# Optimization experiments

Hardware: AMD Instinct MI355X
Metric: run time of the kernel (lower is better)

Reference implementation:

```python
import jax, jax.numpy as jnp
import numpy as np
import math

HIDDEN = 1024
HEADS = 16
HEAD = HIDDEN // HEADS  # 64
SCALE_BASE = 512.0


def _gammas(heads):
    # 1 - exp(linspace(log(1/32), log(1/512), heads))
    return 1.0 - jnp.exp(jnp.linspace(math.log(1.0 / 32.0), math.log(1.0 / 512.0), heads))


def _xpos(x, downscale):
    # x: [B, H, S, d]  (same head_size d for every head -> shared tables)
    S, d = x.shape[2], x.shape[3]
    half = d // 2
    base_scale = (jnp.arange(0, d, 2, dtype=jnp.float32) + 0.4 * d) / (1.4 * d)  # [half]
    pos = jnp.arange(S, dtype=jnp.float32)
    scale = base_scale[None, :] ** (pos / SCALE_BASE)[:, None]  # [S, half]
    if downscale:
        scale = 1.0 / scale
    inv_freq = 1.0 / (10000.0 ** (jnp.arange(half, dtype=jnp.float32) / half))
    sinusoid = pos[:, None] * inv_freq[None, :]  # [S, half]
    # duplicate-interleave (each column repeated twice)
    sin = jnp.repeat(jnp.sin(sinusoid) * scale, 2, axis=-1)  # [S, d]
    cos = jnp.repeat(jnp.cos(sinusoid) * scale, 2, axis=-1)  # [S, d]
    x1 = x[..., ::2]
    x2 = x[..., 1::2]
    rot = jnp.stack([-x2, x1], axis=-1).reshape(x.shape)  # rotate_every_two
    return x * cos + rot * sin


def _decay_mask(S, gammas):
    # D[h, n, m] = gamma_h^(n-m) for n >= m else 0
    n = jnp.arange(S)[:, None]
    m = jnp.arange(S)[None, :]
    diff = (n - m).astype(jnp.float32)
    mask = (n >= m)
    pw = jnp.maximum(diff, 0.0)[None, :, :]  # avoid overflow on negative diffs
    return jnp.where(mask[None, :, :], gammas[:, None, None] ** pw, 0.0)  # [H, S, S]


def retention_forward(Q, K, V):
    B, S, _ = Q.shape
    # split heads: [B, S, HIDDEN] -> [B, H, S, HEAD]
    def split(x, hd):
        return x.reshape(B, S, HEADS, hd).transpose(0, 2, 1, 3)
    q = _xpos(split(Q, HEAD), downscale=False)
    k = _xpos(split(K, HEAD), downscale=True)
    v = split(V, HEAD)
    D = _decay_mask(S, _gammas(HEADS).astype(Q.dtype))  # [H, S, S]
    scores = jnp.einsum('bhsd,bhtd->bhst', q, k) * D[None]
    out = jnp.einsum('bhst,bhtd->bhsd', scores, v)
    return out.transpose(0, 2, 1, 3).reshape(B, S, HEADS * HEAD)


def setup_inputs() -> dict:
    key = jax.random.key(0)
    kq, kk, kv = jax.random.split(key, 3)
    B, S = 2, 2048
    return {
        'Q': jax.random.normal(kq, (B, S, HIDDEN), dtype=jnp.float32),
        'K': jax.random.normal(kk, (B, S, HIDDEN), dtype=jnp.float32),
        'V': jax.random.normal(kv, (B, S, HIDDEN), dtype=jnp.float32),
    }


def reference(Q, K, V):
    return retention_forward(Q, K, V)
```

## Files before the change

kernel.cpp:

```cpp
#include <hip/hip_runtime.h>
#include <hip/hip_bf16.h>
#include <math.h>

#define B_  2
#define S_  2048
#define H_  16
#define D_  64

typedef __attribute__((ext_vector_type(8))) short bf16x8_t;
typedef __attribute__((ext_vector_type(4))) float f32x4_t;

__device__ __forceinline__ unsigned short f2bf(float f) {
    __hip_bfloat16 h = __float2bfloat16(f);
    return __builtin_bit_cast(unsigned short, h);
}
__device__ __forceinline__ float bf2f(unsigned short u) {
    unsigned int x = ((unsigned int)u) << 16;
    return __builtin_bit_cast(float, x);
}

__device__ __forceinline__ void rotpair(int i, float pos, float& cs_s, float& sn_s, bool down) {
    float bsc  = (2.0f * (float)i + 25.6f) / 89.6f;
    float xsc  = exp2f(log2f(bsc) * pos * (1.0f / 512.0f));
    float invf = exp2f(-(float)i * (13.287712379549449f / 32.0f));
    float ang  = pos * invf;
    float kq = rintf(ang * 0.15915494309189535f);
    float rr = fmaf(kq, -6.2831853071795865f, ang);
    float sn = sinf(rr), cs = cosf(rr);
    float sc = down ? (1.0f / xsc) : xsc;
    cs_s = cs * sc; sn_s = sn * sc;
}

__global__ __launch_bounds__(256) void gkv_kernel(const float* __restrict__ K,
                                                  const float* __restrict__ V,
                                                  unsigned short* __restrict__ kb,
                                                  unsigned short* __restrict__ vt,
                                                  unsigned short* __restrict__ Gg) {
    __shared__ float tileF[64 * 65];
    __shared__ __align__(16) unsigned short vtile[64 * 72];
    __shared__ __align__(16) unsigned short ktile[64 * 72];
    int t = threadIdx.x;
    int idx = blockIdx.x;
    int bh = idx >> 5, j = idx & 31;
    int b = bh >> 4, hh = bh & 15;
    int s0 = j * 64;
    int d = t >> 2, c = t & 3;

    float lnv = -3.4657359027997265f + (float)hh * (-0.18483924814931874f);
    float l2g = log2f(1.0f - expf(lnv));

    float4 vreg[4];
#pragma unroll
    for (int it = 0; it < 4; ++it) {
        int f  = it * 256 + t;
        int sl = f >> 4, d4 = f & 15;
        vreg[it] = *(const float4*)(V + ((long)(b * S_ + s0 + sl)) * 1024 + hh * 64 + d4 * 4);
    }
    float kreg[4][4];
#pragma unroll
    for (int it = 0; it < 4; ++it) {
        int f  = it * 256 + t;
        int sl = f >> 4, d4 = f & 15;
        float pos = (float)(s0 + sl);
        long a = ((long)(b * S_ + s0 + sl)) * 1024 + hh * 64 + d4 * 4;
        float4 xk = *(const float4*)(K + a);
        float gsi = exp2f(-pos * l2g);
        float c0, s0f, c1, s1f;
        rotpair(2 * d4 + 0, pos, c0, s0f, true);
        rotpair(2 * d4 + 1, pos, c1, s1f, true);
        float ck0 = c0 * gsi, sk0 = s0f * gsi;
        float ck1 = c1 * gsi, sk1 = s1f * gsi;
        kreg[it][0] = xk.x * ck0 - xk.y * sk0;
        kreg[it][1] = xk.y * ck0 + xk.x * sk0;
        kreg[it][2] = xk.z * ck1 - xk.w * sk1;
        kreg[it][3] = xk.w * ck1 + xk.z * sk1;
        *(uint2*)(kb + a) = make_uint2((unsigned)f2bf(kreg[it][0]) | ((unsigned)f2bf(kreg[it][1]) << 16),
                                       (unsigned)f2bf(kreg[it][2]) | ((unsigned)f2bf(kreg[it][3]) << 16));
    }
#pragma unroll
    for (int it = 0; it < 4; ++it) {
        int f  = it * 256 + t;
        int sl = f >> 4, d4 = f & 15;
        tileF[sl * 65 + d4 * 4 + 0] = vreg[it].x;
        tileF[sl * 65 + d4 * 4 + 1] = vreg[it].y;
        tileF[sl * 65 + d4 * 4 + 2] = vreg[it].z;
        tileF[sl * 65 + d4 * 4 + 3] = vreg[it].w;
    }
    __syncthreads();
    {
        unsigned int pk[8];
#pragma unroll
        for (int jj = 0; jj < 8; ++jj) {
            float f0 = tileF[(c * 16 + 2 * jj + 0) * 65 + d];
            float f1 = tileF[(c * 16 + 2 * jj + 1) * 65 + d];
            pk[jj] = (unsigned int)f2bf(f0) | ((unsigned int)f2bf(f1) << 16);
        }
        uint4 u0 = make_uint4(pk[0], pk[1], pk[2], pk[3]);
        uint4 u1 = make_uint4(pk[4], pk[5], pk[6], pk[7]);
        ((uint4*)&vtile[d * 72 + c * 16])[0] = u0;
        ((uint4*)&vtile[d * 72 + c * 16 + 8])[0] = u1;
        unsigned short* outp = vt + ((long)(bh * 64 + d)) * S_ + s0 + c * 16;
        ((uint4*)outp)[0] = u0;
        ((uint4*)outp)[1] = u1;
    }
    __syncthreads();
#pragma unroll
    for (int it = 0; it < 4; ++it) {
        int f  = it * 256 + t;
        int sl = f >> 4, d4 = f & 15;
        tileF[sl * 65 + d4 * 4 + 0] = kreg[it][0];
        tileF[sl * 65 + d4 * 4 + 1] = kreg[it][1];
        tileF[sl * 65 + d4 * 4 + 2] = kreg[it][2];
        tileF[sl * 65 + d4 * 4 + 3] = kreg[it][3];
    }
    __syncthreads();
    {
        unsigned int pk[8];
#pragma unroll
        for (int jj = 0; jj < 8; ++jj) {
            float f0 = tileF[(c * 16 + 2 * jj + 0) * 65 + d];
            float f1 = tileF[(c * 16 + 2 * jj + 1) * 65 + d];
            pk[jj] = (unsigned int)f2bf(f0) | ((unsigned int)f2bf(f1) << 16);
        }
        ((uint4*)&ktile[d * 72 + c * 16])[0] = make_uint4(pk[0], pk[1], pk[2], pk[3]);
        ((uint4*)&ktile[d * 72 + c * 16 + 8])[0] = make_uint4(pk[4], pk[5], pk[6], pk[7]);
    }
    __syncthreads();

    int w = t >> 6, lane = t & 63, quad = lane >> 4, l16 = lane & 15;
    f32x4_t accS[4];
#pragma unroll
    for (int dkt = 0; dkt < 4; ++dkt) accS[dkt] = (f32x4_t){0.f, 0.f, 0.f, 0.f};

    bf16x8_t aV[2], bK[4][2];
#pragma unroll
    for (int sst = 0; sst < 2; ++sst)
        aV[sst] = *(const bf16x8_t*)&vtile[(w * 16 + l16) * 72 + sst * 32 + quad * 8];
#pragma unroll
    for (int dkt = 0; dkt < 4; ++dkt)
#pragma unroll
        for (int sst = 0; sst < 2; ++sst)
            bK[dkt][sst] = *(const bf16x8_t*)&ktile[(dkt * 16 + l16) * 72 + sst * 32 + quad * 8];
#pragma unroll
    for (int dkt = 0; dkt < 4; ++dkt)
#pragma unroll
        for (int sst = 0; sst < 2; ++sst)
            accS[dkt] = __builtin_amdgcn_mfma_f32_16x16x32_bf16(aV[sst], bK[dkt][sst], accS[dkt], 0, 0, 0);

    unsigned short* Gp = Gg + (long)idx * 4096;
#pragma unroll
    for (int dkt = 0; dkt < 4; ++dkt)
#pragma unroll
        for (int r = 0; r < 4; ++r)
            Gp[(w * 16 + quad * 4 + r) * 64 + dkt * 16 + l16] = f2bf(accS[dkt][r]);
}

__global__ __launch_bounds__(256) void scan_kernel(const unsigned short* __restrict__ Gg,
                                                   unsigned short* __restrict__ Sg) {
    int tid = blockIdx.x * 256 + threadIdx.x;
    int bh  = tid >> 12;
    int e   = tid & 4095;
    long base = ((long)bh * 32) * 4096 + e;
    float acc = 0.0f;
#pragma unroll
    for (int j = 0; j < 32; ++j) {
        if (j > 0) Sg[base + (long)j * 4096] = f2bf(acc);
        acc += bf2f(Gg[base + (long)j * 4096]);
    }
}

__global__ __launch_bounds__(256) void outc_kernel(const float* __restrict__ Q,
                                                   const unsigned short* __restrict__ kb,
                                                   const unsigned short* __restrict__ vt,
                                                   const unsigned short* __restrict__ Sg,
                                                   float* __restrict__ out) {
    __shared__ __align__(16) unsigned short strip[4][16 * 72];
    int t = threadIdx.x;
    int w = t >> 6, lane = t & 63, quad = lane >> 4, l16 = lane & 15;
    int idx = blockIdx.x;
    int bh  = idx & 31;
    int tch = idx >> 5;
    int b = bh >> 4, hh = bh & 15;

    const unsigned short* kB = kb + ((long)(b * S_ + tch * 64)) * 1024 + hh * 64;
    const unsigned short* vB = vt + (long)bh * 64 * S_ + tch * 64;
    const unsigned short* SB = Sg + ((long)(bh * 32 + tch)) * 4096;

    float lnv = -3.4657359027997265f + (float)hh * (-0.18483924814931874f);
    float l2g = log2f(1.0f - expf(lnv));
    int qrow = w * 16 + l16;
    float pos = (float)(tch * 64 + qrow);
    float gs = exp2f(pos * l2g);
    const float* Qp = Q + ((long)(b * S_ + tch * 64 + qrow)) * 1024 + hh * 64;

    bf16x8_t aQ[2];
#pragma unroll
    for (int kk = 0; kk < 2; ++kk) {
        int d0 = kk * 32 + quad * 8;
        float4 x0 = *(const float4*)(Qp + d0);
        float4 x1 = *(const float4*)(Qp + d0 + 4);
        float xs0 = x0.x, xs1 = x0.y, xs2 = x0.z, xs3 = x0.w;
        float xs4 = x1.x, xs5 = x1.y, xs6 = x1.z, xs7 = x1.w;
        bf16x8_t q;
#pragma unroll
        for (int p = 0; p < 4; ++p) {
            float cv, sv;
            rotpair(d0 / 2 + p, pos, cv, sv, false);
            float cq = cv * gs, sq = sv * gs;
            float xe = (p == 0) ? xs0 : (p == 1) ? xs2 : (p == 2) ? xs4 : xs6;
            float xo = (p == 0) ? xs1 : (p == 1) ? xs3 : (p == 2) ? xs5 : xs7;
            q[2 * p]     = (short)f2bf(xe * cq - xo * sq);
            q[2 * p + 1] = (short)f2bf(xo * cq + xe * sq);
        }
        aQ[kk] = q;
    }

    f32x4_t accO[4];
#pragma unroll
    for (int dvt = 0; dvt < 4; ++dvt) accO[dvt] = (f32x4_t){0.f, 0.f, 0.f, 0.f};

    if (tch > 0) {
#pragma unroll
        for (int dvt = 0; dvt < 4; ++dvt)
#pragma unroll
            for (int kk = 0; kk < 2; ++kk) {
                bf16x8_t bS = *(const bf16x8_t*)(SB + (dvt * 16 + l16) * 64 + kk * 32 + quad * 8);
                accO[dvt] = __builtin_amdgcn_mfma_f32_16x16x32_bf16(aQ[kk], bS, accO[dvt], 0, 0, 0);
            }
    }

    unsigned short* sw = strip[w];
    for (int st = w + 1; st < 4; ++st)
        *(uint2*)&sw[l16 * 72 + st * 16 + quad * 4] = make_uint2(0u, 0u);

    for (int st = 0; st <= w; ++st) {
        f32x4_t pp = (f32x4_t){0.f, 0.f, 0.f, 0.f};
#pragma unroll
        for (int kk = 0; kk < 2; ++kk) {
            bf16x8_t aK = *(const bf16x8_t*)(kB + (long)(st * 16 + l16) * 1024 + kk * 32 + quad * 8);
            pp = __builtin_amdgcn_mfma_f32_16x16x32_bf16(aK, aQ[kk], pp, 0, 0, 0);
        }
        if (st == w) {
#pragma unroll
            for (int r = 0; r < 4; ++r)
                if (quad * 4 + r > l16) pp[r] = 0.0f;
        }
        uint2 pk2;
        pk2.x = (unsigned)f2bf(pp[0]) | ((unsigned)f2bf(pp[1]) << 16);
        pk2.y = (unsigned)f2bf(pp[2]) | ((unsigned)f2bf(pp[3]) << 16);
        *(uint2*)&sw[l16 * 72 + st * 16 + quad * 4] = pk2;
    }

    bf16x8_t aP0 = *(const bf16x8_t*)&sw[l16 * 72 + 0 * 32 + quad * 8];
#pragma unroll
    for (int dvt = 0; dvt < 4; ++dvt) {
        bf16x8_t bV0 = *(const bf16x8_t*)(vB + (long)(dvt * 16 + l16) * S_ + 0 * 32 + quad * 8);
        accO[dvt] = __builtin_amdgcn_mfma_f32_16x16x32_bf16(aP0, bV0, accO[dvt], 0, 0, 0);
    }
    if (w >= 2) {
        bf16x8_t aP1 = *(const bf16x8_t*)&sw[l16 * 72 + 1 * 32 + quad * 8];
#pragma unroll
        for (int dvt = 0; dvt < 4; ++dvt) {
            bf16x8_t bV1 = *(const bf16x8_t*)(vB + (long)(dvt * 16 + l16) * S_ + 1 * 32 + quad * 8);
            accO[dvt] = __builtin_amdgcn_mfma_f32_16x16x32_bf16(aP1, bV1, accO[dvt], 0, 0, 0);
        }
    }

#pragma unroll
    for (int dvt = 0; dvt < 4; ++dvt)
#pragma unroll
        for (int r = 0; r < 4; ++r) {
            int row = tch * 64 + w * 16 + quad * 4 + r;
            out[((long)(b * S_ + row)) * 1024 + hh * 64 + dvt * 16 + l16] = accO[dvt][r];
        }
}

extern "C" void kernel_launch(void* const* d_in, const int* in_sizes, int n_in,
                              void* d_out, int out_size, void* d_ws, size_t ws_size,
                              hipStream_t stream) {
    const float* Q = (const float*)d_in[0];
    const float* K = (const float*)d_in[1];
    const float* V = (const float*)d_in[2];
    float* out = (float*)d_out;

    const size_t perBuf = (size_t)B_ * H_ * S_ * D_;
    unsigned short* kb = (unsigned short*)d_ws;
    unsigned short* vt = kb + perBuf;
    unsigned short* Sg = vt + perBuf;
    unsigned short* Gg = Sg + perBuf;

    hipLaunchKernelGGL(gkv_kernel,  dim3(1024), dim3(256), 0, stream, K, V, kb, vt, Gg);
    hipLaunchKernelGGL(scan_kernel, dim3(512),  dim3(256), 0, stream, Gg, Sg);
    hipLaunchKernelGGL(outc_kernel, dim3(1024), dim3(256), 0, stream, Q, kb, vt, Sg, out);
}
```

Measured before the change: 112.0 us.

## Fuse prefix-scan of chunk states into output kernel, drop scan launch

Removes the separate scan kernel and its Sg buffer. Each output block now sums the preceding chunk states from Gg into shared memory itself and reads the MFMA operands from LDS. Block order is reversed so the most expensive chunks, which sum the most states, are scheduled first. This saves a launch and the Sg write/read round trip, but adds redundant O(chunks^2) reads of Gg across blocks, mostly served from L2.

New measurement: 113.1 us. Within noise of the previous version (+1.0%).

```diff
diff --git a/kernel.cpp b/kernel.cpp
--- a/kernel.cpp
+++ b/kernel.cpp
@@ -155,36 +155,22 @@
             Gp[(w * 16 + quad * 4 + r) * 64 + dkt * 16 + l16] = f2bf(accS[dkt][r]);
 }
 
-__global__ __launch_bounds__(256) void scan_kernel(const unsigned short* __restrict__ Gg,
-                                                   unsigned short* __restrict__ Sg) {
-    int tid = blockIdx.x * 256 + threadIdx.x;
-    int bh  = tid >> 12;
-    int e   = tid & 4095;
-    long base = ((long)bh * 32) * 4096 + e;
-    float acc = 0.0f;
-#pragma unroll
-    for (int j = 0; j < 32; ++j) {
-        if (j > 0) Sg[base + (long)j * 4096] = f2bf(acc);
-        acc += bf2f(Gg[base + (long)j * 4096]);
-    }
-}
-
 __global__ __launch_bounds__(256) void outc_kernel(const float* __restrict__ Q,
                                                    const unsigned short* __restrict__ kb,
                                                    const unsigned short* __restrict__ vt,
-                                                   const unsigned short* __restrict__ Sg,
+                                                   const unsigned short* __restrict__ Gg,
                                                    float* __restrict__ out) {
     __shared__ __align__(16) unsigned short strip[4][16 * 72];
+    __shared__ __align__(16) unsigned short Sld[64 * 72];
     int t = threadIdx.x;
     int w = t >> 6, lane = t & 63, quad = lane >> 4, l16 = lane & 15;
     int idx = blockIdx.x;
     int bh  = idx & 31;
-    int tch = idx >> 5;
+    int tch = 31 - (idx >> 5);
     int b = bh >> 4, hh = bh & 15;
 
     const unsigned short* kB = kb + ((long)(b * S_ + tch * 64)) * 1024 + hh * 64;
     const unsigned short* vB = vt + (long)bh * 64 * S_ + tch * 64;
-    const unsigned short* SB = Sg + ((long)(bh * 32 + tch)) * 4096;
 
     float lnv = -3.4657359027997265f + (float)hh * (-0.18483924814931874f);
     float l2g = log2f(1.0f - expf(lnv));
@@ -215,6 +201,32 @@
         aQ[kk] = q;
     }
 
+    if (tch > 0) {
+        const unsigned short* Gb = Gg + ((long)bh * 32) * 4096;
+        int ebase = t * 16;
+        float acc[16];
+#pragma unroll
+        for (int e = 0; e < 16; ++e) acc[e] = 0.0f;
+        for (int jj = 0; jj < tch; ++jj) {
+            const uint4* src = (const uint4*)(Gb + (long)jj * 4096 + ebase);
+            uint4 u0 = src[0], u1 = src[1];
+            unsigned int uu[8] = {u0.x, u0.y, u0.z, u0.w, u1.x, u1.y, u1.z, u1.w};
+#pragma unroll
+            for (int h = 0; h < 8; ++h) {
+                acc[2 * h]     += bf2f((unsigned short)(uu[h] & 0xffff));
+                acc[2 * h + 1] += bf2f((unsigned short)(uu[h] >> 16));
+            }
+        }
+        unsigned int pk[8];
+#pragma unroll
+        for (int h = 0; h < 8; ++h)
+            pk[h] = (unsigned)f2bf(acc[2 * h]) | ((unsigned)f2bf(acc[2 * h + 1]) << 16);
+        uint4* dst = (uint4*)&Sld[(t >> 2) * 72 + (t & 3) * 16];
+        dst[0] = make_uint4(pk[0], pk[1], pk[2], pk[3]);
+        dst[1] = make_uint4(pk[4], pk[5], pk[6], pk[7]);
+    }
+    __syncthreads();
+
     f32x4_t accO[4];
 #pragma unroll
     for (int dvt = 0; dvt < 4; ++dvt) accO[dvt] = (f32x4_t){0.f, 0.f, 0.f, 0.f};
@@ -224,7 +236,7 @@
         for (int dvt = 0; dvt < 4; ++dvt)
 #pragma unroll
             for (int kk = 0; kk < 2; ++kk) {
-                bf16x8_t bS = *(const bf16x8_t*)(SB + (dvt * 16 + l16) * 64 + kk * 32 + quad * 8);
+                bf16x8_t bS = *(const bf16x8_t*)&Sld[(dvt * 16 + l16) * 72 + kk * 32 + quad * 8];
                 accO[dvt] = __builtin_amdgcn_mfma_f32_16x16x32_bf16(aQ[kk], bS, accO[dvt], 0, 0, 0);
             }
     }
@@ -286,10 +298,8 @@
     const size_t perBuf = (size_t)B_ * H_ * S_ * D_;
     unsigned short* kb = (unsigned short*)d_ws;
     unsigned short* vt = kb + perBuf;
-    unsigned short* Sg = vt + perBuf;
-    unsigned short* Gg = Sg + perBuf;
+    unsigned short* Gg = vt + perBuf;
 
     hipLaunchKernelGGL(gkv_kernel,  dim3(1024), dim3(256), 0, stream, K, V, kb, vt, Gg);
-    hipLaunchKernelGGL(scan_kernel, dim3(512),  dim3(256), 0, stream, Gg, Sg);
-    hipLaunchKernelGGL(outc_kernel, dim3(1024), dim3(256), 0, stream, Q, kb, vt, Sg, out);
-}
+    hipLaunchKernelGGL(outc_kernel, dim3(1024), dim3(256), 0, stream, Q, kb, vt, Gg, out);
+}
```
